# Kernel tuning notes

Measured on AMD Instinct MI355X. Metric: run time of the kernel, lower is better.

The kernel has to match this reference:

```python
import jax, jax.numpy as jnp
import numpy as np

N = 50000   # nodes
E = 800000  # edges
D = 256     # in = hidden = out channels
R = 16      # num_relations (last index reserved for self-loops)
B = 8       # num_bases
LN_EPS = 1e-5


def setup_inputs() -> dict:
    key = jax.random.key(0)
    ks = jax.random.split(key, 20)
    s_basis = np.sqrt(2.0 / (D + D)).astype(np.float32)  # glorot-ish scale
    s_att = np.sqrt(2.0 / (R + B)).astype(np.float32)
    inp = {
        "x": jax.random.normal(ks[0], (N, D), dtype=jnp.float32),
        "edge_index": jax.random.randint(ks[1], (2, E), 0, N),
        "edge_type": jax.random.randint(ks[2], (E,), 0, R),
        "edge_attr": jax.random.uniform(ks[3], (E,), dtype=jnp.float32),
        # layer 1 params
        "basis1": jax.random.normal(ks[4], (B, D, D), dtype=jnp.float32) * s_basis,
        "att1": jax.random.normal(ks[5], (R, B), dtype=jnp.float32) * s_att,
        "root1": jax.random.normal(ks[6], (D, D), dtype=jnp.float32) * s_basis,
        "bias1": jnp.zeros((D,), dtype=jnp.float32),
        "ln1_g": jnp.ones((D,), dtype=jnp.float32),
        "ln1_b": jnp.zeros((D,), dtype=jnp.float32),
        # layer 2 params
        "basis2": jax.random.normal(ks[7], (B, D, D), dtype=jnp.float32) * s_basis,
        "att2": jax.random.normal(ks[8], (R, B), dtype=jnp.float32) * s_att,
        "root2": jax.random.normal(ks[9], (D, D), dtype=jnp.float32) * s_basis,
        "bias2": jnp.zeros((D,), dtype=jnp.float32),
        "ln2_g": jnp.ones((D,), dtype=jnp.float32),
        "ln2_b": jnp.zeros((D,), dtype=jnp.float32),
    }
    return inp


def _layer_norm(x, g, b):
    mu = jnp.mean(x, axis=-1, keepdims=True)
    var = jnp.mean(jnp.square(x - mu), axis=-1, keepdims=True)
    return (x - mu) * jax.lax.rsqrt(var + LN_EPS) * g + b


def _rgcn_layer(x, edge_index, edge_type, edge_attr, basis, att, root, bias):
    n = x.shape[0]
    r = att.shape[0]
    # W_r = sum_b a_rb V_b ; then per-relation transform of every node.
    weight = jnp.einsum('rb,bio->rio', att, basis)          # [R, D, D]
    H = jnp.einsum('ni,rio->nro', x, weight)                # [N, R, D]
    # append self-loops with relation index R-1 and confidence 1.0
    loop = jnp.arange(n, dtype=edge_index.dtype)
    src = jnp.concatenate([edge_index[0], loop])
    dst = jnp.concatenate([edge_index[1], loop])
    et = jnp.concatenate([edge_type, jnp.full((n,), r - 1, dtype=edge_type.dtype)])
    ea = jnp.concatenate([edge_attr, jnp.ones((n,), dtype=x.dtype)])
    msg = H[src, et] * ea[:, None]                          # [E+N, D]
    summ = jax.ops.segment_sum(msg, dst, num_segments=n)
    cnt = jax.ops.segment_sum(jnp.ones_like(ea), dst, num_segments=n)
    agg = summ / cnt[:, None]                               # scatter-mean (cnt >= 1 via self-loops)
    return agg + x @ root + bias


def reference(x, edge_index, edge_type, edge_attr,
              basis1, att1, root1, bias1, ln1_g, ln1_b,
              basis2, att2, root2, bias2, ln2_g, ln2_b):
    # input_proj / output_proj are Identity since in == hidden == out.
    h = x
    h_out = _rgcn_layer(h, edge_index, edge_type, edge_attr, basis1, att1, root1, bias1)
    h = jax.nn.relu(_layer_norm(h + h_out, ln1_g, ln1_b))
    h_out = _rgcn_layer(h, edge_index, edge_type, edge_attr, basis2, att2, root2, bias2)
    h = jax.nn.relu(_layer_norm(h + h_out, ln2_g, ln2_b))
    return h
```

## Files before the change

kernel.cpp:

```cpp
#include <hip/hip_runtime.h>
#include <stdint.h>

#define D 256
#define RREL 16
#define BB 8
#define K9 2304
#define KG 2048
#define LN_EPS 1e-5f
#define NT (K9 / 64)
#define BUFB 49152

typedef __attribute__((ext_vector_type(8))) short frag8;
typedef __attribute__((ext_vector_type(4))) float floatx4;
typedef __attribute__((ext_vector_type(2))) float float2v;

__device__ __forceinline__ unsigned short f2bf(float f) {
    union { float f; uint32_t u; } v; v.f = f;
    uint32_t r = (v.u + 0x7FFFu + ((v.u >> 16) & 1u)) >> 16;
    return (unsigned short)r;
}
__device__ __forceinline__ float bf2f(unsigned short u) {
    union { uint32_t u; float f; } v; v.u = (uint32_t)u << 16;
    return v.f;
}
__device__ __forceinline__ float2v bfpair(uint32_t d) {
    union { uint32_t u; float f; } lo, hi;
    lo.u = d << 16; hi.u = d & 0xFFFF0000u;
    return (float2v){lo.f, hi.f};
}

__device__ __forceinline__ float2v pk_mul(float2v a, float2v b) {
    float2v d;
    asm("v_pk_mul_f32 %0, %1, %2" : "=v"(d) : "v"(a), "v"(b));
    return d;
}
__device__ __forceinline__ void pk_fma_lo(float2v& acc, float2v c, float2v x) {
    asm("v_pk_fma_f32 %0, %1, %2, %0 op_sel:[0,0,0] op_sel_hi:[1,0,1]"
        : "+v"(acc) : "v"(c), "v"(x));
}
__device__ __forceinline__ void pk_fma_hi(float2v& acc, float2v c, float2v x) {
    asm("v_pk_fma_f32 %0, %1, %2, %0 op_sel:[0,1,0] op_sel_hi:[1,1,1]"
        : "+v"(acc) : "v"(c), "v"(x));
}

__device__ __forceinline__ void gl2lds16(const unsigned short* g, char* l) {
    __builtin_amdgcn_global_load_lds((const __attribute__((address_space(1))) void*)g,
                                     (__attribute__((address_space(3))) void*)l, 16, 0, 0);
}

__global__ __launch_bounds__(256) void k_cvt(const float* __restrict__ src,
                                             unsigned short* __restrict__ dst, int n4) {
    int i = blockIdx.x * 256 + threadIdx.x;
    if (i >= n4) return;
    float4 v = ((const float4*)src)[i];
    ushort4 o = make_ushort4(f2bf(v.x), f2bf(v.y), f2bf(v.z), f2bf(v.w));
    ((ushort4*)dst)[i] = o;
}

__global__ __launch_bounds__(256) void k_deg(const int* __restrict__ ei,
                                             int* __restrict__ deg, int E) {
    int t = blockIdx.x * 256 + threadIdx.x;
    int stride = gridDim.x * 256;
    int d[8];
#pragma unroll
    for (int j = 0; j < 8; ++j) {
        int e = t + j * stride;
        d[j] = (e < E) ? ei[E + e] : -1;
    }
#pragma unroll
    for (int j = 0; j < 8; ++j)
        if (d[j] >= 0) atomicAdd(&deg[d[j]], 1);
}

__global__ __launch_bounds__(256) void k_scan1(const int* __restrict__ deg,
                                               int* __restrict__ csum, int N) {
    __shared__ int sh[256];
    int n = blockIdx.x * 256 + threadIdx.x;
    sh[threadIdx.x] = (n < N) ? deg[n] : 0;
    __syncthreads();
    for (int off = 128; off > 0; off >>= 1) {
        if (threadIdx.x < off) sh[threadIdx.x] += sh[threadIdx.x + off];
        __syncthreads();
    }
    if (threadIdx.x == 0) csum[blockIdx.x] = sh[0];
}

__global__ __launch_bounds__(256) void k_scan3(const int* __restrict__ deg,
                                               const int* __restrict__ csum, int nch,
                                               int* __restrict__ rowptr,
                                               int* __restrict__ cursor,
                                               float* __restrict__ cnt, int N) {
    __shared__ int sh[256];
    int tid = threadIdx.x;
    int bid = blockIdx.x;
    int base;
    if (nch <= 256) {
        int c = (tid < nch) ? csum[tid] : 0;
        sh[tid] = c;
        __syncthreads();
        for (int off = 1; off < 256; off <<= 1) {
            int t = (tid >= off) ? sh[tid - off] : 0;
            __syncthreads();
            sh[tid] += t;
            __syncthreads();
        }
        base = sh[bid] - csum[bid];
        if (bid == 0 && tid == 255) rowptr[N] = sh[255];
        __syncthreads();
    } else {
        int s = 0;
        for (int i = 0; i < bid; ++i) s += csum[i];
        base = s;
        if (bid == 0 && tid == 0) {
            int tot = 0;
            for (int i = 0; i < nch; ++i) tot += csum[i];
            rowptr[N] = tot;
        }
    }
    int n = bid * 256 + tid;
    int v = (n < N) ? deg[n] : 0;
    sh[tid] = v;
    __syncthreads();
    for (int off = 1; off < 256; off <<= 1) {
        int t = (tid >= off) ? sh[tid - off] : 0;
        __syncthreads();
        sh[tid] += t;
        __syncthreads();
    }
    int excl = sh[tid] - v + base;
    if (n < N) {
        rowptr[n] = excl;
        cursor[n] = excl;
        cnt[n] = (float)(v + 1);
    }
}

__global__ __launch_bounds__(256) void k_scatter(const int* __restrict__ ei,
                                                 const int* __restrict__ et,
                                                 const float* __restrict__ ea,
                                                 int* __restrict__ cursor,
                                                 int2* __restrict__ ep, int E) {
    int t = blockIdx.x * 256 + threadIdx.x;
    int stride = gridDim.x * 256;
    int src[8], dst[8], typ[8]; float w[8]; bool v[8];
#pragma unroll
    for (int j = 0; j < 8; ++j) {
        int e = t + j * stride;
        v[j] = (e < E);
        if (v[j]) { src[j] = ei[e]; dst[j] = ei[E + e]; typ[j] = et[e]; w[j] = ea[e]; }
    }
    int p[8];
#pragma unroll
    for (int j = 0; j < 8; ++j)
        if (v[j]) p[j] = atomicAdd(&cursor[dst[j]], 1);
#pragma unroll
    for (int j = 0; j < 8; ++j)
        if (v[j]) ep[p[j]] = make_int2(src[j] | (typ[j] << 24), __float_as_int(w[j]));
}

__global__ __launch_bounds__(256) void k_prep_w(const float* __restrict__ basis,
                                                const float* __restrict__ root,
                                                unsigned short* __restrict__ Wt) {
    __shared__ float tile[64][65];
    int k0 = blockIdx.x * 64, o0 = blockIdx.y * 64;
    const float* src = (k0 < BB * D) ? (basis + (size_t)k0 * D)
                                     : (root + (size_t)(k0 - BB * D) * D);
    int tid = threadIdx.x;
#pragma unroll
    for (int t = 0; t < 16; ++t) {
        int idx = t * 256 + tid;
        int kk = idx >> 6, oo = idx & 63;
        tile[kk][oo] = src[(size_t)kk * D + o0 + oo];
    }
    __syncthreads();
#pragma unroll
    for (int t = 0; t < 16; ++t) {
        int idx = t * 256 + tid;
        int oo = idx >> 6, kk = idx & 63;
        Wt[(size_t)(o0 + oo) * K9 + k0 + kk] = f2bf(tile[kk][oo]);
    }
}

__device__ __forceinline__ void edge_fma(float2v g2[4][4], float2v c0, float2v c1,
                                         float2v c2, float2v c3,
                                         float2v x0, float2v x1) {
    pk_fma_lo(g2[0][0], c0, x0); pk_fma_lo(g2[1][0], c1, x0);
    pk_fma_lo(g2[2][0], c2, x0); pk_fma_lo(g2[3][0], c3, x0);
    pk_fma_hi(g2[0][1], c0, x0); pk_fma_hi(g2[1][1], c1, x0);
    pk_fma_hi(g2[2][1], c2, x0); pk_fma_hi(g2[3][1], c3, x0);
    pk_fma_lo(g2[0][2], c0, x1); pk_fma_lo(g2[1][2], c1, x1);
    pk_fma_lo(g2[2][2], c2, x1); pk_fma_lo(g2[3][2], c3, x1);
    pk_fma_hi(g2[0][3], c0, x1); pk_fma_hi(g2[1][3], c1, x1);
    pk_fma_hi(g2[2][3], c2, x1); pk_fma_hi(g2[3][3], c3, x1);
}

__device__ __forceinline__ void do_edge(float2v g2[4][4], const float* att_s,
                                        int2 pe, uint2 ud) {
    int r = (unsigned)pe.x >> 24;
    const float4* Ar = (const float4*)&att_s[r * BB];
    float4 a0 = Ar[0], a1 = Ar[1];
    float we = __int_as_float(pe.y);
    float2v w2 = {we, we};
    float2v c0 = pk_mul(w2, (float2v){a0.x, a0.y});
    float2v c1 = pk_mul(w2, (float2v){a0.z, a0.w});
    float2v c2 = pk_mul(w2, (float2v){a1.x, a1.y});
    float2v c3 = pk_mul(w2, (float2v){a1.z, a1.w});
    float2v x0 = bfpair(ud.x), x1 = bfpair(ud.y);
    edge_fma(g2, c0, c1, c2, c3, x0, x1);
}

__global__ __launch_bounds__(256) void k_gather(
    const unsigned short* __restrict__ xb, const float* __restrict__ att,
    const int* __restrict__ rowptr, const int2* __restrict__ ep,
    const float* __restrict__ cnt,
    unsigned short* __restrict__ G, int n0, int rows, int N) {
    __shared__ __align__(32) float att_s[RREL * BB];
    int tid = threadIdx.x;
    if (tid < RREL * BB) att_s[tid] = att[tid];
    __syncthreads();
    int wv = tid >> 6, lane = tid & 63;
    int rloc = blockIdx.x * 4 + wv;
    if (rloc >= rows) return;
    int n = n0 + rloc;
    unsigned short* gout = G + (size_t)rloc * KG + lane * 4;
    if (n >= N) {
        ushort4 z = make_ushort4(0, 0, 0, 0);
#pragma unroll
        for (int b = 0; b < BB; ++b) *(ushort4*)(gout + b * D) = z;
        return;
    }
    uint2 xu = *(const uint2*)&xb[(size_t)n * D + lane * 4];
    float2v xs0 = bfpair(xu.x), xs1 = bfpair(xu.y);
    float xv[4] = {xs0.x, xs0.y, xs1.x, xs1.y};

    float2v g2[4][4];
#pragma unroll
    for (int bp = 0; bp < 4; ++bp) {
        float2v ap = {att_s[(RREL - 1) * BB + 2 * bp],
                      att_s[(RREL - 1) * BB + 2 * bp + 1]};
#pragma unroll
        for (int j = 0; j < 4; ++j) {
            float2v xs = {xv[j], xv[j]};
            g2[bp][j] = ap * xs;
        }
    }

    int e0 = rowptr[n], e1 = rowptr[n + 1];
    int e = e0;
    for (; e + 4 <= e1; e += 4) {
        int2 pa = ep[e], pb = ep[e + 1], pc = ep[e + 2], pd = ep[e + 3];
        uint2 uA = *(const uint2*)&xb[(size_t)(pa.x & 0xFFFFFF) * D + lane * 4];
        uint2 uB = *(const uint2*)&xb[(size_t)(pb.x & 0xFFFFFF) * D + lane * 4];
        uint2 uC = *(const uint2*)&xb[(size_t)(pc.x & 0xFFFFFF) * D + lane * 4];
        uint2 uD = *(const uint2*)&xb[(size_t)(pd.x & 0xFFFFFF) * D + lane * 4];
        __builtin_amdgcn_sched_barrier(0);
        do_edge(g2, att_s, pa, uA);
        do_edge(g2, att_s, pb, uB);
        do_edge(g2, att_s, pc, uC);
        do_edge(g2, att_s, pd, uD);
    }
    if (e + 2 <= e1) {
        int2 pa = ep[e], pb = ep[e + 1];
        uint2 uA = *(const uint2*)&xb[(size_t)(pa.x & 0xFFFFFF) * D + lane * 4];
        uint2 uB = *(const uint2*)&xb[(size_t)(pb.x & 0xFFFFFF) * D + lane * 4];
        __builtin_amdgcn_sched_barrier(0);
        do_edge(g2, att_s, pa, uA);
        do_edge(g2, att_s, pb, uB);
        e += 2;
    }
    if (e < e1) {
        int2 pa = ep[e];
        uint2 uA = *(const uint2*)&xb[(size_t)(pa.x & 0xFFFFFF) * D + lane * 4];
        do_edge(g2, att_s, pa, uA);
    }
    float inv = 1.0f / cnt[n];
    float2v inv2 = {inv, inv};
#pragma unroll
    for (int bp = 0; bp < 4; ++bp) {
        float2v v0 = pk_mul(inv2, g2[bp][0]);
        float2v v1 = pk_mul(inv2, g2[bp][1]);
        float2v v2 = pk_mul(inv2, g2[bp][2]);
        float2v v3 = pk_mul(inv2, g2[bp][3]);
        ushort4 o0 = make_ushort4(f2bf(v0.x), f2bf(v1.x), f2bf(v2.x), f2bf(v3.x));
        *(ushort4*)(gout + (2 * bp) * D) = o0;
        ushort4 o1 = make_ushort4(f2bf(v0.y), f2bf(v1.y), f2bf(v2.y), f2bf(v3.y));
        *(ushort4*)(gout + (2 * bp + 1) * D) = o1;
    }
}

__global__ __launch_bounds__(1024, 4) void k_gemm(
    const unsigned short* __restrict__ G, const unsigned short* __restrict__ xb,
    const unsigned short* __restrict__ Wt,
    const float* __restrict__ hinf, const unsigned short* __restrict__ hinb,
    const float* __restrict__ bias, const float* __restrict__ gln,
    const float* __restrict__ bln, float* __restrict__ hout,
    unsigned short* __restrict__ houtb, int n0, int N) {
    __shared__ __align__(16) char smem[2 * BUFB];
    float* ps   = (float*)smem;
    float* pq   = ps + 512;
    float* mu_s = ps + 1024;
    float* rs_s = ps + 1152;

    int tid = threadIdx.x;
    int wv = tid >> 6, lane = tid & 63;
    int quad = lane >> 4, l16 = lane & 15;
    int wm = wv >> 2, wn = wv & 3;
    int grow = blockIdx.x * 128;
    int nb = n0 + grow;

    int arow_s = tid >> 3, aslot_s = tid & 7;
    int swzA = (aslot_s ^ (arow_s & 7)) << 3;
    const unsigned short* gAG = G + (size_t)(grow + arow_s) * KG + swzA;
    const unsigned short* gAX = xb + (size_t)(nb + arow_s) * D + swzA;
    char* lA = smem + (tid << 4);
    const unsigned short* gB[2]; char* lB[2];
#pragma unroll
    for (int t = 0; t < 2; ++t) {
        int c = t * 1024 + tid;
        int brow = c >> 3, bslot = c & 7;
        gB[t] = Wt + (size_t)brow * K9 + ((bslot ^ (brow & 7)) << 3);
        lB[t] = smem + 16384 + (c << 4);
    }

    floatx4 acc[2][4];
#pragma unroll
    for (int mf = 0; mf < 2; ++mf)
#pragma unroll
        for (int nf = 0; nf < 4; ++nf)
            acc[mf][nf] = (floatx4){0.f, 0.f, 0.f, 0.f};

    auto STAGE = [&](int it, int soff) {
        const unsigned short* sa =
            (it < 32) ? (gAG + it * 64) : (gAX + (it - 32) * 64);
        gl2lds16(sa, lA + soff);
        int koff = it * 64;
        gl2lds16(gB[0] + koff, lB[0] + soff);
        gl2lds16(gB[1] + koff, lB[1] + soff);
    };
    auto COMPUTE = [&](int soff) {
        const char* Ab = smem + soff;
        const char* Bb = Ab + 16384;
#pragma unroll
        for (int kc = 0; kc < 2; ++kc) {
            int g = kc * 4 + quad;
            frag8 a[2], b[4];
#pragma unroll
            for (int mf = 0; mf < 2; ++mf) {
                int arow = wm * 32 + mf * 16 + l16;
                a[mf] = *(const frag8*)(Ab + arow * 128 + ((g ^ (arow & 7)) << 4));
            }
#pragma unroll
            for (int nf = 0; nf < 4; ++nf) {
                int brow = wn * 64 + nf * 16 + l16;
                b[nf] = *(const frag8*)(Bb + brow * 128 + ((g ^ (brow & 7)) << 4));
            }
#pragma unroll
            for (int mf = 0; mf < 2; ++mf)
#pragma unroll
                for (int nf = 0; nf < 4; ++nf)
                    acc[mf][nf] = __builtin_amdgcn_mfma_f32_16x16x32_bf16(
                        a[mf], b[nf], acc[mf][nf], 0, 0, 0);
        }
    };

    STAGE(0, 0);
    __syncthreads();
    for (int it = 0; it < NT; it += 2) {
        STAGE(it + 1, BUFB);
        COMPUTE(0);
        __syncthreads();
        if (it + 2 < NT) STAGE(it + 2, 0);
        COMPUTE(BUFB);
        __syncthreads();
    }

    int col[4]; float bic[4];
#pragma unroll
    for (int nf = 0; nf < 4; ++nf) {
        col[nf] = wn * 64 + nf * 16 + l16;
        bic[nf] = bias[col[nf]];
    }
#pragma unroll
    for (int mf = 0; mf < 2; ++mf) {
#pragma unroll
        for (int r = 0; r < 4; ++r) {
            int row = wm * 32 + mf * 16 + quad * 4 + r;
            int n = nb + row;
            float s = 0.f, sq = 0.f;
            if (n < N) {
                const float* hpf = hinf ? hinf + (size_t)n * D : nullptr;
                const unsigned short* hpb = hinb ? hinb + (size_t)n * D : nullptr;
#pragma unroll
                for (int nf = 0; nf < 4; ++nf) {
                    float res = hpf ? hpf[col[nf]] : bf2f(hpb[col[nf]]);
                    float v = acc[mf][nf][r] + res + bic[nf];
                    acc[mf][nf][r] = v;
                    s += v; sq += v * v;
                }
            }
            s += __shfl_xor(s, 1); sq += __shfl_xor(sq, 1);
            s += __shfl_xor(s, 2); sq += __shfl_xor(sq, 2);
            s += __shfl_xor(s, 4); sq += __shfl_xor(sq, 4);
            s += __shfl_xor(s, 8); sq += __shfl_xor(sq, 8);
            if (l16 == 0) {
                ps[row * 4 + wn] = s;
                pq[row * 4 + wn] = sq;
            }
        }
    }
    __syncthreads();
    if (tid < 128) {
        float s  = ps[tid * 4] + ps[tid * 4 + 1] + ps[tid * 4 + 2] + ps[tid * 4 + 3];
        float sq = pq[tid * 4] + pq[tid * 4 + 1] + pq[tid * 4 + 2] + pq[tid * 4 + 3];
        float mu = s * (1.f / D);
        mu_s[tid] = mu;
        rs_s[tid] = rsqrtf(sq * (1.f / D) - mu * mu + LN_EPS);
    }
    __syncthreads();

    float gc[4], bc[4];
#pragma unroll
    for (int nf = 0; nf < 4; ++nf) {
        gc[nf] = gln[col[nf]];
        bc[nf] = bln[col[nf]];
    }
#pragma unroll
    for (int mf = 0; mf < 2; ++mf) {
#pragma unroll
        for (int r = 0; r < 4; ++r) {
            int row = wm * 32 + mf * 16 + quad * 4 + r;
            int n = nb + row;
            if (n >= N) continue;
            float mu = mu_s[row], rs = rs_s[row];
#pragma unroll
            for (int nf = 0; nf < 4; ++nf) {
                float o = fmaxf((acc[mf][nf][r] - mu) * rs * gc[nf] + bc[nf], 0.f);
                if (hout)  hout[(size_t)n * D + col[nf]] = o;
                if (houtb) houtb[(size_t)n * D + col[nf]] = f2bf(o);
            }
        }
    }
}

extern "C" void kernel_launch(void* const* d_in, const int* in_sizes, int n_in,
                              void* d_out, int out_size, void* d_ws, size_t ws_size,
                              hipStream_t stream) {
    const float* x      = (const float*)d_in[0];
    const int*   ei     = (const int*)d_in[1];
    const int*   et     = (const int*)d_in[2];
    const float* ea     = (const float*)d_in[3];
    const float* basis1 = (const float*)d_in[4];
    const float* att1   = (const float*)d_in[5];
    const float* root1  = (const float*)d_in[6];
    const float* bias1  = (const float*)d_in[7];
    const float* g1     = (const float*)d_in[8];
    const float* b1     = (const float*)d_in[9];
    const float* basis2 = (const float*)d_in[10];
    const float* att2   = (const float*)d_in[11];
    const float* root2  = (const float*)d_in[12];
    const float* bias2  = (const float*)d_in[13];
    const float* g2     = (const float*)d_in[14];
    const float* b2     = (const float*)d_in[15];
    float* out = (float*)d_out;

    int N = in_sizes[0] / D;
    int E = in_sizes[2];
    int nch = (N + 255) / 256;
    int Mp = ((N + 63) / 64) * 64;
    int T = Mp / 64;
    int Tpad = (T + 1) & ~1;

    char* p = (char*)d_ws;
    size_t used = 0;
    auto alloc = [&](size_t bytes) {
        char* q = p;
        size_t a = (bytes + 255) & ~(size_t)255;
        p += a; used += a;
        return q;
    };
    unsigned short* xb     = (unsigned short*)alloc((size_t)N * D * 2);
    unsigned short* h1b    = (unsigned short*)alloc((size_t)N * D * 2);
    unsigned short* Wt     = (unsigned short*)alloc((size_t)K9 * D * 2);
    int*            deg    = (int*)alloc((size_t)N * 4);
    int*            rowptr = (int*)alloc((size_t)(N + 1) * 4);
    int*            cursor = (int*)alloc((size_t)N * 4);
    float*          cnt    = (float*)alloc((size_t)N * 4);
    int2*           ep     = (int2*)alloc((size_t)E * 8);
    int*            csum   = (int*)alloc((size_t)nch * 4);

    size_t tile_bytes = (size_t)64 * KG * 2;
    size_t remain = (ws_size > used + 256) ? (ws_size - used - 256) : 0;

    float* h1 = nullptr;
    int ct;
    if (remain >= (size_t)Tpad * tile_bytes) {
        ct = Tpad;
    } else {
        h1 = (float*)alloc((size_t)N * D * 4);
        remain = (ws_size > used + 256) ? (ws_size - used - 256) : 0;
        int ct_max = (int)(remain / tile_bytes);
        if (ct_max < 2) ct_max = 2;
        if (ct_max > Tpad) ct_max = Tpad;
        int nch2 = (Tpad + ct_max - 1) / ct_max;
        ct = (Tpad + nch2 - 1) / nch2;
        ct = (ct + 1) & ~1;
        if (ct > ct_max) ct = ct_max & ~1;
        if (ct < 2) ct = 2;
    }
    unsigned short* G = (unsigned short*)alloc((size_t)ct * tile_bytes);

    hipMemsetAsync(deg, 0, (size_t)N * 4, stream);
    int gE8 = (E + 2047) / 2048;
    k_deg<<<gE8, 256, 0, stream>>>(ei, deg, E);
    k_scan1<<<nch, 256, 0, stream>>>(deg, csum, N);
    k_scan3<<<nch, 256, 0, stream>>>(deg, csum, nch, rowptr, cursor, cnt, N);
    k_scatter<<<gE8, 256, 0, stream>>>(ei, et, ea, cursor, ep, E);
    k_cvt<<<(N * D / 4 + 255) / 256, 256, 0, stream>>>(x, xb, N * D / 4);

    const float* bas[2]  = {basis1, basis2};
    const float* attp[2] = {att1, att2};
    const float* rt[2]   = {root1, root2};
    const float* bi[2]   = {bias1, bias2};
    const float* lg[2]   = {g1, g2};
    const float* lb[2]   = {b1, b2};
    const unsigned short* gin[2] = {xb, h1b};
    const float*          hrf[2] = {x, h1};
    const unsigned short* hrb[2] = {nullptr, h1 ? nullptr : h1b};
    float*          hof[2] = {h1, out};
    unsigned short* hob[2] = {h1b, nullptr};

    for (int L = 0; L < 2; ++L) {
        k_prep_w<<<dim3(K9 / 64, D / 64), 256, 0, stream>>>(bas[L], rt[L], Wt);
        for (int c0 = 0; c0 < Tpad; c0 += ct) {
            int tiles = (Tpad - c0 < ct) ? (Tpad - c0) : ct;
            int rows = tiles * 64;
            int n0 = c0 * 64;
            k_gather<<<rows / 4, 256, 0, stream>>>(gin[L], attp[L], rowptr, ep,
                                                   cnt, G, n0, rows, N);
            k_gemm<<<rows / 128, 1024, 0, stream>>>(G, gin[L], Wt, hrf[L], hrb[L],
                                                    bi[L], lg[L], lb[L], hof[L],
                                                    hob[L], n0, N);
        }
    }
}
```

Baseline: 618.2 us.

## Overlap gather of second half with GEMM of first half in one kernel

When the workspace can hold the whole gather buffer, the node rows are split into two halves. A combined kernel runs the GEMM for the first half alongside the gather for the second half, using block-index dispatch, so the memory-bound gather overlaps the compute-bound GEMM. This removes one serialized gather/GEMM boundary per layer. The cost is an extra launch, gather blocks running at 1024 threads with the GEMM's large shared-memory allocation (which may lower occupancy), and possible contention between the two workloads.

```diff
diff --git a/kernel.cpp b/kernel.cpp
--- a/kernel.cpp
+++ b/kernel.cpp
@@ -209,18 +209,11 @@
     edge_fma(g2, c0, c1, c2, c3, x0, x1);
 }
 
-__global__ __launch_bounds__(256) void k_gather(
-    const unsigned short* __restrict__ xb, const float* __restrict__ att,
+__device__ __forceinline__ void gather_node(
+    const float* att_s, const unsigned short* __restrict__ xb,
     const int* __restrict__ rowptr, const int2* __restrict__ ep,
-    const float* __restrict__ cnt,
-    unsigned short* __restrict__ G, int n0, int rows, int N) {
-    __shared__ __align__(32) float att_s[RREL * BB];
-    int tid = threadIdx.x;
-    if (tid < RREL * BB) att_s[tid] = att[tid];
-    __syncthreads();
-    int wv = tid >> 6, lane = tid & 63;
-    int rloc = blockIdx.x * 4 + wv;
-    if (rloc >= rows) return;
+    const float* __restrict__ cnt, unsigned short* __restrict__ G,
+    int n0, int rloc, int N, int lane) {
     int n = n0 + rloc;
     unsigned short* gout = G + (size_t)rloc * KG + lane * 4;
     if (n >= N) {
@@ -288,14 +281,29 @@
     }
 }
 
-__global__ __launch_bounds__(1024, 4) void k_gemm(
+__global__ __launch_bounds__(256) void k_gather(
+    const unsigned short* __restrict__ xb, const float* __restrict__ att,
+    const int* __restrict__ rowptr, const int2* __restrict__ ep,
+    const float* __restrict__ cnt,
+    unsigned short* __restrict__ G, int n0, int rows, int N) {
+    __shared__ __align__(32) float att_s[RREL * BB];
+    int tid = threadIdx.x;
+    if (tid < RREL * BB) att_s[tid] = att[tid];
+    __syncthreads();
+    int wv = tid >> 6, lane = tid & 63;
+    int rloc = blockIdx.x * 4 + wv;
+    if (rloc >= rows) return;
+    gather_node(att_s, xb, rowptr, ep, cnt, G, n0, rloc, N, lane);
+}
+
+__device__ __forceinline__ void gemm_body(
+    char* smem, int bid,
     const unsigned short* __restrict__ G, const unsigned short* __restrict__ xb,
     const unsigned short* __restrict__ Wt,
     const float* __restrict__ hinf, const unsigned short* __restrict__ hinb,
     const float* __restrict__ bias, const float* __restrict__ gln,
     const float* __restrict__ bln, float* __restrict__ hout,
     unsigned short* __restrict__ houtb, int n0, int N) {
-    __shared__ __align__(16) char smem[2 * BUFB];
     float* ps   = (float*)smem;
     float* pq   = ps + 512;
     float* mu_s = ps + 1024;
@@ -305,7 +313,7 @@
     int wv = tid >> 6, lane = tid & 63;
     int quad = lane >> 4, l16 = lane & 15;
     int wm = wv >> 2, wn = wv & 3;
-    int grow = blockIdx.x * 128;
+    int grow = bid * 128;
     int nb = n0 + grow;
 
     int arow_s = tid >> 3, aslot_s = tid & 7;
@@ -439,6 +447,46 @@
                 if (houtb) houtb[(size_t)n * D + col[nf]] = f2bf(o);
             }
         }
+    }
+}
+
+__global__ __launch_bounds__(1024, 4) void k_gemm(
+    const unsigned short* __restrict__ G, const unsigned short* __restrict__ xb,
+    const unsigned short* __restrict__ Wt,
+    const float* __restrict__ hinf, const unsigned short* __restrict__ hinb,
+    const float* __restrict__ bias, const float* __restrict__ gln,
+    const float* __restrict__ bln, float* __restrict__ hout,
+    unsigned short* __restrict__ houtb, int n0, int N) {
+    __shared__ __align__(16) char smem[2 * BUFB];
+    gemm_body(smem, blockIdx.x, G, xb, Wt, hinf, hinb, bias, gln, bln,
+              hout, houtb, n0, N);
+}
+
+__global__ __launch_bounds__(1024, 4) void k_both(
+    const unsigned short* __restrict__ GA, const unsigned short* __restrict__ xb,
+    const unsigned short* __restrict__ Wt,
+    const float* __restrict__ hinf, const unsigned short* __restrict__ hinb,
+    const float* __restrict__ bias, const float* __restrict__ gln,
+    const float* __restrict__ bln, float* __restrict__ hout,
+    unsigned short* __restrict__ houtb, int n0A,
+    const float* __restrict__ att, const int* __restrict__ rowptr,
+    const int2* __restrict__ ep, const float* __restrict__ cnt,
+    unsigned short* __restrict__ GB, int n0B, int rowsB,
+    int N, int ngemm) {
+    __shared__ __align__(16) char smem[2 * BUFB];
+    int bid = blockIdx.x;
+    if (bid < ngemm) {
+        gemm_body(smem, bid, GA, xb, Wt, hinf, hinb, bias, gln, bln,
+                  hout, houtb, n0A, N);
+    } else {
+        float* att_s = (float*)smem;
+        int tid = threadIdx.x;
+        if (tid < RREL * BB) att_s[tid] = att[tid];
+        __syncthreads();
+        int wv = tid >> 6, lane = tid & 63;
+        int rloc = (bid - ngemm) * 16 + wv;
+        if (rloc >= rowsB) return;
+        gather_node(att_s, xb, rowptr, ep, cnt, GB, n0B, rloc, N, lane);
     }
 }
 
@@ -492,8 +540,12 @@
     size_t remain = (ws_size > used + 256) ? (ws_size - used - 256) : 0;
 
     float* h1 = nullptr;
-    int ct;
-    if (remain >= (size_t)Tpad * tile_bytes) {
+    bool pipelined = (remain >= (size_t)Tpad * tile_bytes);
+    int ct0 = 0, ct1 = 0, ct = 0;
+    if (pipelined) {
+        ct0 = ((Tpad / 2) + 1) & ~1;
+        ct1 = Tpad - ct0;
+        if (ct1 <= 0) { ct0 = Tpad; ct1 = 0; pipelined = false; }
         ct = Tpad;
     } else {
         h1 = (float*)alloc((size_t)N * D * 4);
@@ -529,17 +581,38 @@
     float*          hof[2] = {h1, out};
     unsigned short* hob[2] = {h1b, nullptr};
 
-    for (int L = 0; L < 2; ++L) {
-        k_prep_w<<<dim3(K9 / 64, D / 64), 256, 0, stream>>>(bas[L], rt[L], Wt);
-        for (int c0 = 0; c0 < Tpad; c0 += ct) {
-            int tiles = (Tpad - c0 < ct) ? (Tpad - c0) : ct;
-            int rows = tiles * 64;
-            int n0 = c0 * 64;
-            k_gather<<<rows / 4, 256, 0, stream>>>(gin[L], attp[L], rowptr, ep,
-                                                   cnt, G, n0, rows, N);
-            k_gemm<<<rows / 128, 1024, 0, stream>>>(G, gin[L], Wt, hrf[L], hrb[L],
-                                                    bi[L], lg[L], lb[L], hof[L],
-                                                    hob[L], n0, N);
-        }
-    }
-}
+    if (pipelined) {
+        int rows0 = ct0 * 64, rows1 = ct1 * 64;
+        unsigned short* G0 = G;
+        unsigned short* G1 = G + (size_t)ct0 * 64 * KG;
+        for (int L = 0; L < 2; ++L) {
+            k_prep_w<<<dim3(K9 / 64, D / 64), 256, 0, stream>>>(bas[L], rt[L], Wt);
+            k_gather<<<rows0 / 4, 256, 0, stream>>>(gin[L], attp[L], rowptr, ep,
+                                                    cnt, G0, 0, rows0, N);
+            int ngemm = rows0 / 128;
+            int ngath = (rows1 + 15) / 16;
+            k_both<<<ngemm + ngath, 1024, 0, stream>>>(
+                G0, gin[L], Wt, hrf[L], hrb[L], bi[L], lg[L], lb[L],
+                hof[L], hob[L], 0,
+                attp[L], rowptr, ep, cnt, G1, rows0, rows1,
+                N, ngemm);
+            k_gemm<<<rows1 / 128, 1024, 0, stream>>>(G1, gin[L], Wt, hrf[L], hrb[L],
+                                                     bi[L], lg[L], lb[L], hof[L],
+                                                     hob[L], rows0, N);
+        }
+    } else {
+        for (int L = 0; L < 2; ++L) {
+            k_prep_w<<<dim3(K9 / 64, D / 64), 256, 0, stream>>>(bas[L], rt[L], Wt);
+            for (int c0 = 0; c0 < Tpad; c0 += ct) {
+                int tiles = (Tpad - c0 < ct) ? (Tpad - c0) : ct;
+                int rows = tiles * 64;
+                int n0 = c0 * 64;
+                k_gather<<<rows / 4, 256, 0, stream>>>(gin[L], attp[L], rowptr, ep,
+                                                       cnt, G, n0, rows, N);
+                k_gemm<<<rows / 128, 1024, 0, stream>>>(G, gin[L], Wt, hrf[L], hrb[L],
+                                                        bi[L], lg[L], lb[L], hof[L],
+                                                        hob[L], n0, N);
+            }
+        }
+    }
+}
```

Result: slower. 649.0 us (+5.0%).
